# Performance work log

Hardware: AMD Instinct MI355X
Metric: run time of the kernel (lower is better)

## Reference

```python
import jax, jax.numpy as jnp
import numpy as np

B, N, C, H = 2, 2048, 1024, 16
D = C // H
SCALE = D ** -0.5


def setup_inputs() -> dict:
    key = jax.random.key(0)
    ks = jax.random.split(key, 4)
    s = 0.02
    return {
        "x": jax.random.normal(ks[0], (B, N, C), dtype=jnp.float32),
        "f": jax.random.normal(ks[1], (B, N, C), dtype=jnp.float32),
        "W_qkv": jax.random.normal(ks[2], (C, 3 * C), dtype=jnp.float32) * s,
        "W_proj": jax.random.normal(ks[3], (C, C), dtype=jnp.float32) * s,
        "b_proj": jnp.zeros((C,), dtype=jnp.float32),
    }


def reference(x, f, W_qkv, W_proj, b_proj):
    b, n, c = x.shape
    h, d = H, c // H
    # qkv projection -> (B,N,3,H,D) -> q,k,v each (B,H,N,D)
    qkv = (x @ W_qkv).reshape(b, n, 3, h, d)
    q = jnp.transpose(qkv[:, :, 0], (0, 2, 1, 3))
    k = jnp.transpose(qkv[:, :, 1], (0, 2, 1, 3))
    v = jnp.transpose(qkv[:, :, 2], (0, 2, 1, 3))
    # full NxN scores, faithful to the original manual MHA
    attn = jax.nn.softmax(jnp.einsum("bhqd,bhkd->bhqk", q, k) * SCALE, axis=-1)
    av = jnp.einsum("bhqk,bhkd->bhqd", attn, v)  # (B,H,N,D)
    # pre-residual output branch
    attn2gcn = jnp.transpose(av, (0, 2, 1, 3)).reshape(b, n, c)
    # residual fuse with f (reshaped per-head in torch; equivalent to flat add)
    fused = attn2gcn + f
    out = fused @ W_proj + b_proj
    return (out, attn2gcn)
```

## Files before the change

kernel.cpp:

```cpp
#include <hip/hip_runtime.h>
#include <hip/hip_bf16.h>

#define OUT1_OFF 4194304
#define QSCALE 0.1803368801111204f

typedef __attribute__((ext_vector_type(8))) short bf16x8;
typedef __attribute__((ext_vector_type(4))) float f32x4;

__device__ __forceinline__ unsigned short f2bf(float x) {
    unsigned u = __float_as_uint(x);
    u += 0x7FFFu + ((u >> 16) & 1u);
    return (unsigned short)(u >> 16);
}

__device__ __forceinline__ void gl2lds16(const unsigned short* g, unsigned short* l) {
    __builtin_amdgcn_global_load_lds(
        (const __attribute__((address_space(1))) unsigned int*)g,
        (__attribute__((address_space(3))) unsigned int*)l, 16, 0, 0);
}

__global__ __launch_bounds__(256) void prep(const float* __restrict__ x,
                                            const float* __restrict__ Wqkv,
                                            const float* __restrict__ Wproj,
                                            unsigned short* __restrict__ xb,
                                            unsigned short* __restrict__ wqkvT,
                                            unsigned short* __restrict__ wprojT) {
    __shared__ float T[64][65];
    const int bid = blockIdx.x, tid = threadIdx.x;
    if (bid < 4096) {
        int i = bid * 256 + tid;
        float4 v = reinterpret_cast<const float4*>(x)[i];
        ushort4 o = make_ushort4(f2bf(v.x), f2bf(v.y), f2bf(v.z), f2bf(v.w));
        reinterpret_cast<ushort4*>(xb)[i] = o;
        return;
    }
    const float* in; unsigned short* out; int Nd, bx, by;
    if (bid < 4864) { int t = bid - 4096; in = Wqkv;  out = wqkvT;  Nd = 3072; bx = t % 48; by = t / 48; }
    else            { int t = bid - 4864; in = Wproj; out = wprojT; Nd = 1024; bx = t % 16; by = t / 16; }
    const int Kd = 1024;
    const int r0 = by * 64, c0 = bx * 64;
    const int tr = tid >> 3, tc = (tid & 7) * 8;
#pragma unroll
    for (int rr = 0; rr < 64; rr += 32) {
        const float4* p = reinterpret_cast<const float4*>(&in[(r0 + tr + rr) * Nd + c0 + tc]);
        float4 v0 = p[0], v1 = p[1];
        T[tr + rr][tc + 0] = v0.x; T[tr + rr][tc + 1] = v0.y;
        T[tr + rr][tc + 2] = v0.z; T[tr + rr][tc + 3] = v0.w;
        T[tr + rr][tc + 4] = v1.x; T[tr + rr][tc + 5] = v1.y;
        T[tr + rr][tc + 6] = v1.z; T[tr + rr][tc + 7] = v1.w;
    }
    __syncthreads();
#pragma unroll
    for (int rr = 0; rr < 64; rr += 32) {
        int orow = tr + rr;
        ushort4 o0 = make_ushort4(f2bf(T[tc + 0][orow]), f2bf(T[tc + 1][orow]),
                                  f2bf(T[tc + 2][orow]), f2bf(T[tc + 3][orow]));
        ushort4 o1 = make_ushort4(f2bf(T[tc + 4][orow]), f2bf(T[tc + 5][orow]),
                                  f2bf(T[tc + 6][orow]), f2bf(T[tc + 7][orow]));
        unsigned short* dst = &out[(c0 + orow) * Kd + r0 + tc];
        *reinterpret_cast<ushort4*>(dst) = o0;
        *reinterpret_cast<ushort4*>(dst + 4) = o1;
    }
}

__global__ __launch_bounds__(256) void gemm_qkv(const unsigned short* __restrict__ A,
                                                const unsigned short* __restrict__ Bt,
                                                unsigned short* __restrict__ qb,
                                                unsigned short* __restrict__ kb,
                                                unsigned short* __restrict__ vtb) {
    __shared__ __align__(16) unsigned short Sh[18432];
    unsigned short* As = Sh;
    unsigned short* Bs = Sh + 8192;
    const int tid = threadIdx.x;
    const int w = tid >> 6, lane = tid & 63, quad = lane >> 4, l15 = lane & 15;
    const int m0 = blockIdx.y * 128, n0 = blockIdx.x * 128;
    const int wm = (w & 1) * 64, wn = (w >> 1) * 64;
    const int nbase = n0 + wn;
    const int t = nbase >> 10;
    const bool qk = (t < 2);
    const int sw = (l15 & 7) << 3;
    f32x4 acc[4][4] = {};
    for (int k0 = 0; k0 < 1024; k0 += 64) {
        __syncthreads();
#pragma unroll
        for (int tt = 0; tt < 4; ++tt) {
            int c = tt * 256 + tid;
            int row = c >> 3, jg = ((c & 7) ^ (row & 7)) * 8;
            gl2lds16(&A[(m0 + row) * 1024 + k0 + jg], &As[c * 8]);
            gl2lds16(&Bt[(n0 + row) * 1024 + k0 + jg], &Bs[c * 8]);
        }
        __syncthreads();
#pragma unroll
        for (int kk = 0; kk < 2; ++kk) {
            bf16x8 af[4], bfr[4];
#pragma unroll
            for (int i = 0; i < 4; ++i)
                af[i] = *reinterpret_cast<const bf16x8*>(
                    &As[(wm + i * 16 + l15) * 64 + ((((kk * 4 + quad) << 3) ^ sw))]);
#pragma unroll
            for (int j = 0; j < 4; ++j)
                bfr[j] = *reinterpret_cast<const bf16x8*>(
                    &Bs[(wn + j * 16 + l15) * 64 + ((((kk * 4 + quad) << 3) ^ sw))]);
            if (qk) {
#pragma unroll
                for (int i = 0; i < 4; ++i)
#pragma unroll
                    for (int j = 0; j < 4; ++j)
                        acc[i][j] = __builtin_amdgcn_mfma_f32_16x16x32_bf16(bfr[j], af[i], acc[i][j], 0, 0, 0);
            } else {
#pragma unroll
                for (int i = 0; i < 4; ++i)
#pragma unroll
                    for (int j = 0; j < 4; ++j)
                        acc[i][j] = __builtin_amdgcn_mfma_f32_16x16x32_bf16(af[i], bfr[j], acc[i][j], 0, 0, 0);
            }
        }
    }
    __syncthreads();
    unsigned short* scr = Sh + w * 4608;
    const int mb = m0 + wm;
    const int b = mb >> 11;
    const int h = (nbase & 1023) >> 6;
    const float sc = (t == 0) ? QSCALE : 1.f;
    if (qk) {
#pragma unroll
        for (int i = 0; i < 4; ++i) {
            int row = i * 16 + l15;
#pragma unroll
            for (int j = 0; j < 4; ++j) {
                unsigned short h0 = f2bf(acc[i][j][0] * sc), h1 = f2bf(acc[i][j][1] * sc);
                unsigned short h2 = f2bf(acc[i][j][2] * sc), h3 = f2bf(acc[i][j][3] * sc);
                uint2 pk = make_uint2((unsigned)h0 | ((unsigned)h1 << 16),
                                      (unsigned)h2 | ((unsigned)h3 << 16));
                *reinterpret_cast<uint2*>(&scr[row * 72 + j * 16 + quad * 4]) = pk;
            }
        }
        asm volatile("s_waitcnt lgkmcnt(0)" ::: "memory");
        unsigned short* dst = (t == 0 ? qb : kb) + (((b * 16 + h) * 2048) + (mb & 2047)) * 64;
#pragma unroll
        for (int p = 0; p < 8; ++p) {
            int idx = p * 64 + lane;
            *reinterpret_cast<uint4*>(&dst[idx * 8]) =
                *reinterpret_cast<const uint4*>(&scr[(idx >> 3) * 72 + (idx & 7) * 8]);
        }
    } else {
        const int kblk = (mb & 2047) >> 6;
#pragma unroll
        for (int i = 0; i < 4; ++i) {
            int slot0 = ((i & 2) << 4) | (quad << 3) | ((i & 1) << 2);
#pragma unroll
            for (int j = 0; j < 4; ++j) {
                unsigned short h0 = f2bf(acc[i][j][0]), h1 = f2bf(acc[i][j][1]);
                unsigned short h2 = f2bf(acc[i][j][2]), h3 = f2bf(acc[i][j][3]);
                uint2 pk = make_uint2((unsigned)h0 | ((unsigned)h1 << 16),
                                      (unsigned)h2 | ((unsigned)h3 << 16));
                *reinterpret_cast<uint2*>(&scr[(j * 16 + l15) * 72 + slot0]) = pk;
            }
        }
        asm volatile("s_waitcnt lgkmcnt(0)" ::: "memory");
        unsigned short* vtile = vtb + (((b * 16 + h) * 32) + kblk) * 4096;
#pragma unroll
        for (int p = 0; p < 8; ++p) {
            int idx = p * 64 + lane;
            *reinterpret_cast<uint4*>(&vtile[idx * 8]) =
                *reinterpret_cast<const uint4*>(&scr[(idx >> 3) * 72 + (idx & 7) * 8]);
        }
    }
}

__global__ __launch_bounds__(256) void attn_kernel(const unsigned short* __restrict__ qb,
                                                   const unsigned short* __restrict__ kb,
                                                   const unsigned short* __restrict__ vtb,
                                                   const float* __restrict__ f,
                                                   float* __restrict__ attn2_out,
                                                   unsigned short* __restrict__ fusedb) {
    __shared__ __align__(16) unsigned short Ksw[2][4096];
    __shared__ __align__(16) unsigned short Vsw[2][4096];
    const int tid = threadIdx.x;
    const int w = tid >> 6, lane = tid & 63, quad = lane >> 4, l15 = lane & 15;
    const int bh = blockIdx.x;
    const int q0 = blockIdx.y * 128 + w * 32;
    const unsigned short* qr = &qb[(bh * 2048 + q0 + l15) * 64 + quad * 8];
    bf16x8 ql0 = *reinterpret_cast<const bf16x8*>(qr);
    bf16x8 ql1 = *reinterpret_cast<const bf16x8*>(qr + 32);
    bf16x8 ql2 = *reinterpret_cast<const bf16x8*>(qr + 1024);
    bf16x8 ql3 = *reinterpret_cast<const bf16x8*>(qr + 1056);
    const unsigned short* kt0 = kb + bh * 131072;
    const unsigned short* vt0 = vtb + bh * 131072;
    const int c0i = tid, c1i = tid + 256;
    const int gu0 = (((c0i & ~7) | ((c0i & 7) ^ ((c0i >> 3) & 7))) << 3);
    const int gu1 = (((c1i & ~7) | ((c1i & 7) ^ ((c1i >> 3) & 7))) << 3);
    const int sw = (l15 & 7) << 3;
    f32x4 O0[4] = {}, O1[4] = {};
    f32x4 asum0 = {}, asum1 = {};
    bf16x8 ones;
#pragma unroll
    for (int j = 0; j < 8; ++j) ones[j] = (short)0x3F80;

#define STAGE(IT, BUF) do { int _toff = (IT) * 4096;                    \
        gl2lds16(kt0 + _toff + gu0, &Ksw[BUF][c0i * 8]);                \
        gl2lds16(vt0 + _toff + gu0, &Vsw[BUF][c0i * 8]);                \
        gl2lds16(kt0 + _toff + gu1, &Ksw[BUF][c1i * 8]);                \
        gl2lds16(vt0 + _toff + gu1, &Vsw[BUF][c1i * 8]); } while (0)

    auto body = [&](int buf) {
        f32x4 Ta[4], Tb[4];
        __builtin_amdgcn_s_setprio(1);
#pragma unroll
        for (int s = 0; s < 4; ++s) {
            const unsigned short* kr = &Ksw[buf][(s * 16 + l15) * 64];
            bf16x8 k0 = *reinterpret_cast<const bf16x8*>(&kr[(quad << 3) ^ sw]);
            bf16x8 k1 = *reinterpret_cast<const bf16x8*>(&kr[((quad + 4) << 3) ^ sw]);
            f32x4 za = {}, zb = {};
            za = __builtin_amdgcn_mfma_f32_16x16x32_bf16(k0, ql0, za, 0, 0, 0);
            za = __builtin_amdgcn_mfma_f32_16x16x32_bf16(k1, ql1, za, 0, 0, 0);
            zb = __builtin_amdgcn_mfma_f32_16x16x32_bf16(k0, ql2, zb, 0, 0, 0);
            zb = __builtin_amdgcn_mfma_f32_16x16x32_bf16(k1, ql3, zb, 0, 0, 0);
            Ta[s] = za; Tb[s] = zb;
        }
        __builtin_amdgcn_s_setprio(0);
        float pa_[4][4], pb_[4][4];
#pragma unroll
        for (int s = 0; s < 4; ++s)
#pragma unroll
            for (int r = 0; r < 4; ++r) {
                pa_[s][r] = __builtin_amdgcn_exp2f(Ta[s][r]);
                pb_[s][r] = __builtin_amdgcn_exp2f(Tb[s][r]);
            }
        uint4 u0, u1, v0u, v1u;
        u0.x = __builtin_amdgcn_perm(__float_as_uint(pa_[0][1]), __float_as_uint(pa_[0][0]), 0x07060302u);
        u0.y = __builtin_amdgcn_perm(__float_as_uint(pa_[0][3]), __float_as_uint(pa_[0][2]), 0x07060302u);
        u0.z = __builtin_amdgcn_perm(__float_as_uint(pa_[1][1]), __float_as_uint(pa_[1][0]), 0x07060302u);
        u0.w = __builtin_amdgcn_perm(__float_as_uint(pa_[1][3]), __float_as_uint(pa_[1][2]), 0x07060302u);
        u1.x = __builtin_amdgcn_perm(__float_as_uint(pa_[2][1]), __float_as_uint(pa_[2][0]), 0x07060302u);
        u1.y = __builtin_amdgcn_perm(__float_as_uint(pa_[2][3]), __float_as_uint(pa_[2][2]), 0x07060302u);
        u1.z = __builtin_amdgcn_perm(__float_as_uint(pa_[3][1]), __float_as_uint(pa_[3][0]), 0x07060302u);
        u1.w = __builtin_amdgcn_perm(__float_as_uint(pa_[3][3]), __float_as_uint(pa_[3][2]), 0x07060302u);
        v0u.x = __builtin_amdgcn_perm(__float_as_uint(pb_[0][1]), __float_as_uint(pb_[0][0]), 0x07060302u);
        v0u.y = __builtin_amdgcn_perm(__float_as_uint(pb_[0][3]), __float_as_uint(pb_[0][2]), 0x07060302u);
        v0u.z = __builtin_amdgcn_perm(__float_as_uint(pb_[1][1]), __float_as_uint(pb_[1][0]), 0x07060302u);
        v0u.w = __builtin_amdgcn_perm(__float_as_uint(pb_[1][3]), __float_as_uint(pb_[1][2]), 0x07060302u);
        v1u.x = __builtin_amdgcn_perm(__float_as_uint(pb_[2][1]), __float_as_uint(pb_[2][0]), 0x07060302u);
        v1u.y = __builtin_amdgcn_perm(__float_as_uint(pb_[2][3]), __float_as_uint(pb_[2][2]), 0x07060302u);
        v1u.z = __builtin_amdgcn_perm(__float_as_uint(pb_[3][1]), __float_as_uint(pb_[3][0]), 0x07060302u);
        v1u.w = __builtin_amdgcn_perm(__float_as_uint(pb_[3][3]), __float_as_uint(pb_[3][2]), 0x07060302u);
        bf16x8 paa0 = __builtin_bit_cast(bf16x8, u0);
        bf16x8 paa1 = __builtin_bit_cast(bf16x8, u1);
        bf16x8 pba0 = __builtin_bit_cast(bf16x8, v0u);
        bf16x8 pba1 = __builtin_bit_cast(bf16x8, v1u);
        asum0 = __builtin_amdgcn_mfma_f32_16x16x32_bf16(paa0, ones, asum0, 0, 0, 0);
        asum0 = __builtin_amdgcn_mfma_f32_16x16x32_bf16(paa1, ones, asum0, 0, 0, 0);
        asum1 = __builtin_amdgcn_mfma_f32_16x16x32_bf16(pba0, ones, asum1, 0, 0, 0);
        asum1 = __builtin_amdgcn_mfma_f32_16x16x32_bf16(pba1, ones, asum1, 0, 0, 0);
        __builtin_amdgcn_s_setprio(1);
#pragma unroll
        for (int c4 = 0; c4 < 4; ++c4) {
            const unsigned short* vr = &Vsw[buf][(c4 * 16 + l15) * 64];
            bf16x8 v0 = *reinterpret_cast<const bf16x8*>(&vr[(quad << 3) ^ sw]);
            bf16x8 v1 = *reinterpret_cast<const bf16x8*>(&vr[((quad + 4) << 3) ^ sw]);
            O0[c4] = __builtin_amdgcn_mfma_f32_16x16x32_bf16(paa0, v0, O0[c4], 0, 0, 0);
            O0[c4] = __builtin_amdgcn_mfma_f32_16x16x32_bf16(paa1, v1, O0[c4], 0, 0, 0);
            O1[c4] = __builtin_amdgcn_mfma_f32_16x16x32_bf16(pba0, v0, O1[c4], 0, 0, 0);
            O1[c4] = __builtin_amdgcn_mfma_f32_16x16x32_bf16(pba1, v1, O1[c4], 0, 0, 0);
        }
        __builtin_amdgcn_s_setprio(0);
    };

    STAGE(0, 0);
    for (int it = 0; it < 32; it += 2) {
        __syncthreads();
        STAGE(it + 1, 1);
        body(0);
        __syncthreads();
        if (it + 2 < 32) STAGE(it + 2, 0);
        body(1);
    }
#undef STAGE

    const int b = bh >> 4, h = bh & 15;
#pragma unroll
    for (int r = 0; r < 4; ++r) {
        float inv0 = 1.f / asum0[r];
        float inv1 = 1.f / asum1[r];
        int tok0 = q0 + quad * 4 + r;
        int base0 = (b * 2048 + tok0) * 1024 + h * 64;
        int base1 = base0 + 16 * 1024;
#pragma unroll
        for (int c4 = 0; c4 < 4; ++c4) {
            int col = c4 * 16 + l15;
            float o0 = O0[c4][r] * inv0;
            attn2_out[base0 + col] = o0;
            fusedb[base0 + col] = f2bf(o0 + f[base0 + col]);
            float o1 = O1[c4][r] * inv1;
            attn2_out[base1 + col] = o1;
            fusedb[base1 + col] = f2bf(o1 + f[base1 + col]);
        }
    }
}

__global__ __launch_bounds__(256) void gemm_proj(const unsigned short* __restrict__ A,
                                                 const unsigned short* __restrict__ Bt,
                                                 const float* __restrict__ bias,
                                                 float* __restrict__ out) {
    __shared__ __align__(16) unsigned short As[8192];
    __shared__ __align__(16) unsigned short Bs[4096];
    const int tid = threadIdx.x;
    const int w = tid >> 6, lane = tid & 63, quad = lane >> 4, l15 = lane & 15;
    const int m0 = blockIdx.y * 128, n0 = blockIdx.x * 64;
    const int wm = (w & 1) * 64, wn = (w >> 1) * 32;
    const int sw = (l15 & 7) << 3;
    f32x4 acc[4][2] = {};
    for (int k0 = 0; k0 < 1024; k0 += 64) {
        __syncthreads();
#pragma unroll
        for (int t = 0; t < 4; ++t) {
            int c = t * 256 + tid;
            int row = c >> 3, jg = ((c & 7) ^ (row & 7)) * 8;
            gl2lds16(&A[(m0 + row) * 1024 + k0 + jg], &As[c * 8]);
            if (t < 2) gl2lds16(&Bt[(n0 + row) * 1024 + k0 + jg], &Bs[c * 8]);
        }
        __syncthreads();
#pragma unroll
        for (int kk = 0; kk < 2; ++kk) {
            bf16x8 af[4], bfr[2];
#pragma unroll
            for (int i = 0; i < 4; ++i)
                af[i] = *reinterpret_cast<const bf16x8*>(
                    &As[(wm + i * 16 + l15) * 64 + ((((kk * 4 + quad) << 3) ^ sw))]);
#pragma unroll
            for (int j = 0; j < 2; ++j)
                bfr[j] = *reinterpret_cast<const bf16x8*>(
                    &Bs[(wn + j * 16 + l15) * 64 + ((((kk * 4 + quad) << 3) ^ sw))]);
#pragma unroll
            for (int i = 0; i < 4; ++i)
#pragma unroll
                for (int j = 0; j < 2; ++j)
                    acc[i][j] = __builtin_amdgcn_mfma_f32_16x16x32_bf16(af[i], bfr[j], acc[i][j], 0, 0, 0);
        }
    }
#pragma unroll
    for (int j = 0; j < 2; ++j) {
        int n = n0 + wn + j * 16 + l15;
        float bv = bias[n];
#pragma unroll
        for (int i = 0; i < 4; ++i)
#pragma unroll
            for (int r = 0; r < 4; ++r) {
                int m = m0 + wm + i * 16 + quad * 4 + r;
                out[m * 1024 + n] = acc[i][j][r] + bv;
            }
    }
}

extern "C" void kernel_launch(void* const* d_in, const int* in_sizes, int n_in,
                              void* d_out, int out_size, void* d_ws, size_t ws_size,
                              hipStream_t stream) {
    const float* x      = (const float*)d_in[0];
    const float* f      = (const float*)d_in[1];
    const float* W_qkv  = (const float*)d_in[2];
    const float* W_proj = (const float*)d_in[3];
    const float* b_proj = (const float*)d_in[4];
    float* out   = (float*)d_out;
    float* attn2 = out + OUT1_OFF;

    char* ws = (char*)d_ws;
    unsigned short* xb     = (unsigned short*)(ws);
    unsigned short* wqkvT  = (unsigned short*)(ws + 8388608);
    unsigned short* wprojT = (unsigned short*)(ws + 14680064);
    unsigned short* qb     = (unsigned short*)(ws + 16777216);
    unsigned short* kb     = (unsigned short*)(ws + 25165824);
    unsigned short* vtb    = (unsigned short*)(ws + 33554432);
    unsigned short* fusedb = (unsigned short*)(ws + 41943040);

    prep<<<5120, 256, 0, stream>>>(x, W_qkv, W_proj, xb, wqkvT, wprojT);
    gemm_qkv<<<dim3(24, 32), 256, 0, stream>>>(xb, wqkvT, qb, kb, vtb);
    attn_kernel<<<dim3(32, 16), 256, 0, stream>>>(qb, kb, vtb, f, attn2, fusedb);
    gemm_proj<<<dim3(16, 32), 256, 0, stream>>>(fusedb, wprojT, b_proj, out);
}
```

Before: 191.9 us.

## Split attention KV range across two wave groups and merge partials in LDS

Measured after the change: 187.0 us. 2.5% less time.

```diff
diff --git a/kernel.cpp b/kernel.cpp
--- a/kernel.cpp
+++ b/kernel.cpp
@@ -168,28 +168,27 @@
     }
 }
 
-__global__ __launch_bounds__(256) void attn_kernel(const unsigned short* __restrict__ qb,
-                                                   const unsigned short* __restrict__ kb,
-                                                   const unsigned short* __restrict__ vtb,
-                                                   const float* __restrict__ f,
-                                                   float* __restrict__ attn2_out,
-                                                   unsigned short* __restrict__ fusedb) {
-    __shared__ __align__(16) unsigned short Ksw[2][4096];
-    __shared__ __align__(16) unsigned short Vsw[2][4096];
+__global__ __launch_bounds__(512, 4) void attn_kernel(const unsigned short* __restrict__ qb,
+                                                      const unsigned short* __restrict__ kb,
+                                                      const unsigned short* __restrict__ vtb,
+                                                      const float* __restrict__ f,
+                                                      float* __restrict__ attn2_out,
+                                                      unsigned short* __restrict__ fusedb) {
+    __shared__ __align__(16) unsigned char SMEM[69632];
+    unsigned short* S16 = reinterpret_cast<unsigned short*>(SMEM);
     const int tid = threadIdx.x;
     const int w = tid >> 6, lane = tid & 63, quad = lane >> 4, l15 = lane & 15;
+    const int qg = w & 3, kh = w >> 2;
     const int bh = blockIdx.x;
-    const int q0 = blockIdx.y * 128 + w * 32;
-    const unsigned short* qr = &qb[(bh * 2048 + q0 + l15) * 64 + quad * 8];
+    const int q0w = blockIdx.y * 128 + qg * 32;
+    const unsigned short* qr = &qb[(bh * 2048 + q0w + l15) * 64 + quad * 8];
     bf16x8 ql0 = *reinterpret_cast<const bf16x8*>(qr);
     bf16x8 ql1 = *reinterpret_cast<const bf16x8*>(qr + 32);
     bf16x8 ql2 = *reinterpret_cast<const bf16x8*>(qr + 1024);
     bf16x8 ql3 = *reinterpret_cast<const bf16x8*>(qr + 1056);
     const unsigned short* kt0 = kb + bh * 131072;
     const unsigned short* vt0 = vtb + bh * 131072;
-    const int c0i = tid, c1i = tid + 256;
-    const int gu0 = (((c0i & ~7) | ((c0i & 7) ^ ((c0i >> 3) & 7))) << 3);
-    const int gu1 = (((c1i & ~7) | ((c1i & 7) ^ ((c1i >> 3) & 7))) << 3);
+    const int gu = (((tid & ~7) | ((tid & 7) ^ ((tid >> 3) & 7))) << 3);
     const int sw = (l15 & 7) << 3;
     f32x4 O0[4] = {}, O1[4] = {};
     f32x4 asum0 = {}, asum1 = {};
@@ -197,18 +196,21 @@
 #pragma unroll
     for (int j = 0; j < 8; ++j) ones[j] = (short)0x3F80;
 
-#define STAGE(IT, BUF) do { int _toff = (IT) * 4096;                    \
-        gl2lds16(kt0 + _toff + gu0, &Ksw[BUF][c0i * 8]);                \
-        gl2lds16(vt0 + _toff + gu0, &Vsw[BUF][c0i * 8]);                \
-        gl2lds16(kt0 + _toff + gu1, &Ksw[BUF][c1i * 8]);                \
-        gl2lds16(vt0 + _toff + gu1, &Vsw[BUF][c1i * 8]); } while (0)
+#define STAGE(IT, BUF) do { unsigned short* db_ = &S16[(BUF) * 16384 + tid * 8]; \
+        const int go_ = (IT) * 4096 + gu;                                        \
+        gl2lds16(kt0 + go_, db_);                                                \
+        gl2lds16(vt0 + go_, db_ + 4096);                                         \
+        gl2lds16(kt0 + 65536 + go_, db_ + 8192);                                 \
+        gl2lds16(vt0 + 65536 + go_, db_ + 12288); } while (0)
 
     auto body = [&](int buf) {
+        const unsigned short* Kb = &S16[buf * 16384 + kh * 8192];
+        const unsigned short* Vb = Kb + 4096;
         f32x4 Ta[4], Tb[4];
         __builtin_amdgcn_s_setprio(1);
 #pragma unroll
         for (int s = 0; s < 4; ++s) {
-            const unsigned short* kr = &Ksw[buf][(s * 16 + l15) * 64];
+            const unsigned short* kr = &Kb[(s * 16 + l15) * 64];
             bf16x8 k0 = *reinterpret_cast<const bf16x8*>(&kr[(quad << 3) ^ sw]);
             bf16x8 k1 = *reinterpret_cast<const bf16x8*>(&kr[((quad + 4) << 3) ^ sw]);
             f32x4 za = {}, zb = {};
@@ -255,7 +257,7 @@
         __builtin_amdgcn_s_setprio(1);
 #pragma unroll
         for (int c4 = 0; c4 < 4; ++c4) {
-            const unsigned short* vr = &Vsw[buf][(c4 * 16 + l15) * 64];
+            const unsigned short* vr = &Vb[(c4 * 16 + l15) * 64];
             bf16x8 v0 = *reinterpret_cast<const bf16x8*>(&vr[(quad << 3) ^ sw]);
             bf16x8 v1 = *reinterpret_cast<const bf16x8*>(&vr[((quad + 4) << 3) ^ sw]);
             O0[c4] = __builtin_amdgcn_mfma_f32_16x16x32_bf16(paa0, v0, O0[c4], 0, 0, 0);
@@ -267,34 +269,60 @@
     };
 
     STAGE(0, 0);
-    for (int it = 0; it < 32; it += 2) {
+    for (int it = 0; it < 16; it += 2) {
         __syncthreads();
         STAGE(it + 1, 1);
         body(0);
         __syncthreads();
-        if (it + 2 < 32) STAGE(it + 2, 0);
+        if (it + 2 < 16) STAGE(it + 2, 0);
         body(1);
     }
 #undef STAGE
 
+    __syncthreads();
+    float* scr = reinterpret_cast<float*>(SMEM);
+    {
+        float* myr = scr + w * 2176;
+#pragma unroll
+        for (int c4 = 0; c4 < 4; ++c4) {
+            int dcol = c4 * 16 + l15;
+#pragma unroll
+            for (int r = 0; r < 4; ++r) {
+                myr[(quad * 4 + r) * 68 + dcol] = O0[c4][r];
+                myr[(16 + quad * 4 + r) * 68 + dcol] = O1[c4][r];
+            }
+        }
+        if (l15 == 0) {
+#pragma unroll
+            for (int r = 0; r < 4; ++r) {
+                myr[(quad * 4 + r) * 68 + 64] = asum0[r];
+                myr[(16 + quad * 4 + r) * 68 + 64] = asum1[r];
+            }
+        }
+    }
+    __syncthreads();
     const int b = bh >> 4, h = bh & 15;
-#pragma unroll
-    for (int r = 0; r < 4; ++r) {
-        float inv0 = 1.f / asum0[r];
-        float inv1 = 1.f / asum1[r];
-        int tok0 = q0 + quad * 4 + r;
-        int base0 = (b * 2048 + tok0) * 1024 + h * 64;
-        int base1 = base0 + 16 * 1024;
-#pragma unroll
-        for (int c4 = 0; c4 < 4; ++c4) {
-            int col = c4 * 16 + l15;
-            float o0 = O0[c4][r] * inv0;
-            attn2_out[base0 + col] = o0;
-            fusedb[base0 + col] = f2bf(o0 + f[base0 + col]);
-            float o1 = O1[c4][r] * inv1;
-            attn2_out[base1 + col] = o1;
-            fusedb[base1 + col] = f2bf(o1 + f[base1 + col]);
-        }
+    const float* rA = scr + qg * 2176;
+    const float* rB = rA + 4 * 2176;
+    const int row = kh * 16 + (lane >> 2);
+    const int dq = (lane & 3) * 16;
+    const int base = (b * 2048 + (q0w + row)) * 1024 + h * 64;
+    const float den = rA[row * 68 + 64] + rB[row * 68 + 64];
+    const float inv = 1.f / den;
+#pragma unroll
+    for (int j = 0; j < 4; ++j) {
+        int d = dq + j * 4;
+        f32x4 pa = *reinterpret_cast<const f32x4*>(&rA[row * 68 + d]);
+        f32x4 pb = *reinterpret_cast<const f32x4*>(&rB[row * 68 + d]);
+        float4 fv = *reinterpret_cast<const float4*>(&f[base + d]);
+        float o0 = (pa[0] + pb[0]) * inv;
+        float o1 = (pa[1] + pb[1]) * inv;
+        float o2 = (pa[2] + pb[2]) * inv;
+        float o3 = (pa[3] + pb[3]) * inv;
+        *reinterpret_cast<float4*>(&attn2_out[base + d]) = make_float4(o0, o1, o2, o3);
+        ushort4 pk = make_ushort4(f2bf(o0 + fv.x), f2bf(o1 + fv.y),
+                                  f2bf(o2 + fv.z), f2bf(o3 + fv.w));
+        *reinterpret_cast<ushort4*>(&fusedb[base + d]) = pk;
     }
 }
 
@@ -374,6 +402,6 @@
 
     prep<<<5120, 256, 0, stream>>>(x, W_qkv, W_proj, xb, wqkvT, wprojT);
     gemm_qkv<<<dim3(24, 32), 256, 0, stream>>>(xb, wqkvT, qb, kb, vtb);
-    attn_kernel<<<dim3(32, 16), 256, 0, stream>>>(qb, kb, vtb, f, attn2, fusedb);
+    attn_kernel<<<dim3(32, 16), 512, 0, stream>>>(qb, kb, vtb, f, attn2, fusedb);
     gemm_proj<<<dim3(16, 32), 256, 0, stream>>>(fusedb, wprojT, b_proj, out);
 }
```
